# Kernel optimization log

Hardware: AMD Instinct MI355X
Metric: run time of the kernel (lower is better)

The kernel has to match this reference:

```python
import jax, jax.numpy as jnp
import numpy as np
import math

B, S, D_MODEL = 4, 2048, 1024
H, D_HEAD = 16, 64
INIT_RANGE = 0.02


def setup_inputs() -> dict:
    key = jax.random.key(0)
    ks = jax.random.split(key, 10)
    x = jax.random.normal(ks[0], (B, S, D_MODEL), dtype=jnp.float32)
    # torch Linear(in,out): y = x @ W.T + b. We store weights pre-transposed as [H, in, out].
    u = lambda k, shape: jax.random.uniform(k, shape, dtype=jnp.float32, minval=-INIT_RANGE, maxval=INIT_RANGE)
    wq = u(ks[1], (H, D_MODEL, D_HEAD))
    wk = u(ks[2], (H, D_MODEL, D_HEAD))
    wv = u(ks[3], (H, D_MODEL, D_HEAD))
    wo = u(ks[4], (H, D_HEAD, D_MODEL))
    # biases: torch default init is uniform(-1/sqrt(fan_in), 1/sqrt(fan_in)); values don't matter for correctness harness
    bq = u(ks[5], (H, D_HEAD))
    bk = u(ks[6], (H, D_HEAD))
    bv = u(ks[7], (H, D_HEAD))
    bo = u(ks[8], (H, D_MODEL))
    return {"normalized_resid_pre": x, "wq": wq, "bq": bq, "wk": wk, "bk": bk,
            "wv": wv, "bv": bv, "wo": wo, "bo": bo}


def reference(normalized_resid_pre, wq, bq, wk, bk, wv, bv, wo, bo):
    x = normalized_resid_pre  # [B, S, D]
    # Batched multi-head QKV projections (original does a python loop per head)
    q = jnp.einsum('bsd,hde->bhse', x, wq) + bq[None, :, None, :]  # [B,H,S,dh]
    k = jnp.einsum('bsd,hde->bhse', x, wk) + bk[None, :, None, :]
    v = jnp.einsum('bsd,hde->bhse', x, wv) + bv[None, :, None, :]
    scale = 1.0 / math.sqrt(D_HEAD)  # cfg.global_d_head, used unconditionally
    scores = jnp.einsum('bhse,bhte->bhst', q, k) * scale  # [B,H,S,S], non-causal
    attn = jax.nn.softmax(scores, axis=-1)
    heads = jnp.einsum('bhst,bhte->bhse', attn, v)  # [B,H,S,dh]
    # per-head output projections, summed over heads (= sum of per-head Linear outputs)
    out = jnp.einsum('bhse,hed->bsd', heads, wo) + jnp.sum(bo, axis=0)[None, None, :]
    return out
```

## Files before the change

### kernel.cpp

```cpp
#include <hip/hip_runtime.h>
#include <hip/hip_bf16.h>
#include <math.h>


typedef __attribute__((ext_vector_type(8))) short bf16x8;
typedef __attribute__((ext_vector_type(4))) float f32x4;

#define GLDS16(gsrc, lbase) \
    __builtin_amdgcn_global_load_lds((const __attribute__((address_space(1))) void*)(gsrc), \
                                     (__attribute__((address_space(3))) void*)(lbase), 16, 0, 0)

static __device__ __forceinline__ ushort f2bf(float f) {
    unsigned u = __float_as_uint(f);
    u += 0x7fff + ((u >> 16) & 1);
    return (ushort)(u >> 16);
}
static __device__ __forceinline__ float clampf(float v) {
    return fminf(fmaxf(v, -1e30f), 1e30f);
}

__global__ void cvt_x(const float* __restrict__ x, ushort* __restrict__ xb) {
    int idx = blockIdx.x * 256 + threadIdx.x;
    float4 a = ((const float4*)x)[idx * 2];
    float4 b = ((const float4*)x)[idx * 2 + 1];
    uint4 o;
    o.x = (unsigned)f2bf(a.x) | ((unsigned)f2bf(a.y) << 16);
    o.y = (unsigned)f2bf(a.z) | ((unsigned)f2bf(a.w) << 16);
    o.z = (unsigned)f2bf(b.x) | ((unsigned)f2bf(b.y) << 16);
    o.w = (unsigned)f2bf(b.z) | ((unsigned)f2bf(b.w) << 16);
    ((uint4*)xb)[idx] = o;
}

__global__ void pack_wqkv(const float* __restrict__ wq, const float* __restrict__ wk,
                          const float* __restrict__ wv, const float* __restrict__ bq,
                          const float* __restrict__ bk, const float* __restrict__ bv,
                          ushort* __restrict__ WT, float* __restrict__ biasc) {
    int idx = blockIdx.x * 256 + threadIdx.x;
    int k = idx & 1023, n = idx >> 10;
    int proj = n >> 10, he = n & 1023, h = he >> 6, e = he & 63;
    const float* w = (proj == 0) ? wq : (proj == 1) ? wk : wv;
    WT[idx] = f2bf(w[(size_t)h * 65536 + (size_t)k * 64 + e]);
    if (k == 0) {
        const float* bb = (proj == 0) ? bq : (proj == 1) ? bk : bv;
        biasc[n] = bb[he];
    }
}
__global__ void pack_wo(const float* __restrict__ wo, const float* __restrict__ bo,
                        ushort* __restrict__ WoT, float* __restrict__ biaso) {
    int idx = blockIdx.x * 256 + threadIdx.x;
    int he = idx & 1023, d = idx >> 10;
    WoT[idx] = f2bf(wo[(size_t)he * 1024 + d]);
    if (he == 0) {
        float s = 0.f;
        for (int hh = 0; hh < 16; ++hh) s += bo[hh * 1024 + d];
        biaso[d] = s;
    }
}

__global__ __launch_bounds__(256, 2) void gemm_bt(
    const ushort* __restrict__ A, const ushort* __restrict__ Bt,
    const float* __restrict__ bias, ushort* __restrict__ C, ushort* __restrict__ Vt,
    float* __restrict__ Cf, int M, int N, int K, int ldc, int n_split)
{
    __shared__ __align__(16) ushort Al[128][64];
    __shared__ __align__(16) ushort Bl[128][64];
    const int t = threadIdx.x;
    const int lane = t & 63, wave = t >> 6;
    const int wr = wave >> 1, wc = wave & 1;
    const int quad = lane >> 4, l16 = lane & 15;
    const int row0 = blockIdx.x * 128, col0 = blockIdx.y * 128;
    const int sr = t >> 3;
    const int scx = ((t & 7) ^ (sr & 7)) * 8;
    const int xk = l16 & 7;

    f32x4 acc[4][4] = {};

    for (int kt = 0; kt < K; kt += 64) {
        char* abase = (char*)Al + wave * 1024;
        char* bbase = (char*)Bl + wave * 1024;
        const ushort* ag = A  + (size_t)(row0 + sr) * K + kt + scx;
        const ushort* bg = Bt + (size_t)(col0 + sr) * K + kt + scx;
        #pragma unroll
        for (int i = 0; i < 4; ++i) {
            GLDS16(ag + (size_t)i * 32 * K, abase + i * 4096);
            GLDS16(bg + (size_t)i * 32 * K, bbase + i * 4096);
        }
        __syncthreads();
        #pragma unroll
        for (int ks = 0; ks < 2; ++ks) {
            bf16x8 a[4], b[4];
            #pragma unroll
            for (int mi = 0; mi < 4; ++mi)
                a[mi] = *(const bf16x8*)(&Al[wr * 64 + mi * 16 + l16][((ks * 4 + quad) ^ xk) * 8]);
            #pragma unroll
            for (int ni = 0; ni < 4; ++ni)
                b[ni] = *(const bf16x8*)(&Bl[wc * 64 + ni * 16 + l16][((ks * 4 + quad) ^ xk) * 8]);
            #pragma unroll
            for (int mi = 0; mi < 4; ++mi)
                #pragma unroll
                for (int ni = 0; ni < 4; ++ni)
                    acc[mi][ni] = __builtin_amdgcn_mfma_f32_16x16x32_bf16(a[mi], b[ni], acc[mi][ni], 0, 0, 0);
        }
        __syncthreads();
    }
    #pragma unroll
    for (int mi = 0; mi < 4; ++mi) {
        int rowb = row0 + wr * 64 + mi * 16 + quad * 4;
        #pragma unroll
        for (int ni = 0; ni < 4; ++ni) {
            int col = col0 + wc * 64 + ni * 16 + l16;
            float bs = bias ? bias[col] : 0.f;
            #pragma unroll
            for (int r = 0; r < 4; ++r) {
                float v = clampf(acc[mi][ni][r] + bs);
                int row = rowb + r;
                if (Cf) {
                    Cf[(size_t)row * ldc + col] = v;
                } else if (col < n_split) {
                    C[(size_t)row * ldc + col] = f2bf(v);
                } else {
                    int bb = row >> 11, s = row & 2047;
                    Vt[(size_t)bb * (1024 * 2048) + (size_t)(col - n_split) * 2048 + s] = f2bf(v);
                }
            }
        }
    }
}

__global__ __launch_bounds__(256, 2) void attn(
    const ushort* __restrict__ QK, const ushort* __restrict__ Vt, ushort* __restrict__ O)
{
    __shared__ __align__(16) ushort Kl[64][64];
    __shared__ __align__(16) ushort Vl[64][64];
    __shared__ ushort Pl[4][32][76];
    const int qt = blockIdx.x, b = blockIdx.y, h = blockIdx.z;
    const int t = threadIdx.x, lane = t & 63, wave = t >> 6;
    const int quad = lane >> 4, l16 = lane & 15;
    const int rowq0 = b * 2048 + qt * 128 + wave * 32;
    const int sr = t >> 3;
    const int scx = ((t & 7) ^ (sr & 7)) * 8;
    const int xk = l16 & 7;
    const float cscale = 0.125f * 1.44269504088896340736f;
    const float M0 = 14.0f;

    bf16x8 qf[2][2];
    #pragma unroll
    for (int mi = 0; mi < 2; ++mi)
        #pragma unroll
        for (int ks = 0; ks < 2; ++ks)
            qf[mi][ks] = *(const bf16x8*)(QK + (size_t)(rowq0 + mi * 16 + l16) * 2048
                                          + h * 64 + ks * 32 + quad * 8);

    f32x4 of[2][4] = {};
    float lpart[2][4] = {};

    for (int kt = 0; kt < 2048; kt += 64) {
        {
            char* kbase = (char*)Kl + wave * 1024;
            char* vbase = (char*)Vl + wave * 1024;
            const ushort* kg = QK + (size_t)(b * 2048 + kt + sr) * 2048 + 1024 + h * 64 + scx;
            const ushort* vg = Vt + (size_t)b * (1024 * 2048) + (size_t)(h * 64 + sr) * 2048 + kt + scx;
            GLDS16(kg, kbase);
            GLDS16(kg + 32 * 2048, kbase + 4096);
            GLDS16(vg, vbase);
            GLDS16(vg + 32 * 2048, vbase + 4096);
        }
        __syncthreads();

        f32x4 sf[2][4] = {};
        #pragma unroll
        for (int ks = 0; ks < 2; ++ks) {
            bf16x8 kb[4];
            #pragma unroll
            for (int nt = 0; nt < 4; ++nt)
                kb[nt] = *(const bf16x8*)(&Kl[nt * 16 + l16][((ks * 4 + quad) ^ xk) * 8]);
            #pragma unroll
            for (int mi = 0; mi < 2; ++mi)
                #pragma unroll
                for (int nt = 0; nt < 4; ++nt)
                    sf[mi][nt] = __builtin_amdgcn_mfma_f32_16x16x32_bf16(qf[mi][ks], kb[nt], sf[mi][nt], 0, 0, 0);
        }

        #pragma unroll
        for (int mi = 0; mi < 2; ++mi) {
            #pragma unroll
            for (int r = 0; r < 4; ++r) {
                float p0 = exp2f(sf[mi][0][r] * cscale - M0);
                float p1 = exp2f(sf[mi][1][r] * cscale - M0);
                float p2 = exp2f(sf[mi][2][r] * cscale - M0);
                float p3 = exp2f(sf[mi][3][r] * cscale - M0);
                lpart[mi][r] += (p0 + p1) + (p2 + p3);
                int prw = mi * 16 + quad * 4 + r;
                Pl[wave][prw][l16 +  0] = f2bf(p0);
                Pl[wave][prw][l16 + 16] = f2bf(p1);
                Pl[wave][prw][l16 + 32] = f2bf(p2);
                Pl[wave][prw][l16 + 48] = f2bf(p3);
            }
        }

        #pragma unroll
        for (int ks = 0; ks < 2; ++ks) {
            bf16x8 pa[2];
            #pragma unroll
            for (int mi = 0; mi < 2; ++mi)
                pa[mi] = *(const bf16x8*)(&Pl[wave][mi * 16 + l16][ks * 32 + quad * 8]);
            #pragma unroll
            for (int nt = 0; nt < 4; ++nt) {
                bf16x8 vb = *(const bf16x8*)(&Vl[nt * 16 + l16][((ks * 4 + quad) ^ xk) * 8]);
                #pragma unroll
                for (int mi = 0; mi < 2; ++mi)
                    of[mi][nt] = __builtin_amdgcn_mfma_f32_16x16x32_bf16(pa[mi], vb, of[mi][nt], 0, 0, 0);
            }
        }
        __syncthreads();
    }

    #pragma unroll
    for (int mi = 0; mi < 2; ++mi) {
        #pragma unroll
        for (int r = 0; r < 4; ++r) {
            float l = lpart[mi][r];
            #pragma unroll
            for (int d = 1; d < 16; d <<= 1) l += __shfl_xor(l, d, 64);
            float inv = 1.0f / fmaxf(l, 1e-30f);
            int row = rowq0 + mi * 16 + quad * 4 + r;
            #pragma unroll
            for (int nt = 0; nt < 4; ++nt)
                O[(size_t)row * 1024 + h * 64 + nt * 16 + l16] = f2bf(clampf(of[mi][nt][r] * inv));
        }
    }
}

extern "C" void kernel_launch(void* const* d_in, const int* in_sizes, int n_in,
                              void* d_out, int out_size, void* d_ws, size_t ws_size,
                              hipStream_t stream) {
    const float* x  = (const float*)d_in[0];
    const float* wq = (const float*)d_in[1];
    const float* bq = (const float*)d_in[2];
    const float* wk = (const float*)d_in[3];
    const float* bk = (const float*)d_in[4];
    const float* wv = (const float*)d_in[5];
    const float* bv = (const float*)d_in[6];
    const float* wo = (const float*)d_in[7];
    const float* bo = (const float*)d_in[8];

    char* ws = (char*)d_ws;
    const size_t MB = 1024 * 1024;
    ushort* xb    = (ushort*)(ws);
    ushort* WqkvT = (ushort*)(ws + 16 * MB);
    ushort* WoT   = (ushort*)(ws + 22 * MB);
    float*  biasc = (float*) (ws + 24 * MB);
    float*  biaso = (float*) (ws + 24 * MB + 64 * 1024);
    ushort* C1    = (ushort*)(ws + 25 * MB);
    ushort* Vt    = (ushort*)(ws + 57 * MB);
    ushort* Obuf  = (ushort*)(ws + 73 * MB);

    cvt_x    <<<4096, 256, 0, stream>>>(x, xb);
    pack_wqkv<<<(3072 * 1024) / 256, 256, 0, stream>>>(wq, wk, wv, bq, bk, bv, WqkvT, biasc);
    pack_wo  <<<(1024 * 1024) / 256, 256, 0, stream>>>(wo, bo, WoT, biaso);

    gemm_bt<<<dim3(64, 24), 256, 0, stream>>>(xb, WqkvT, biasc, C1, Vt, nullptr,
                                              8192, 3072, 1024, 2048, 2048);
    attn<<<dim3(16, 4, 16), 256, 0, stream>>>(C1, Vt, Obuf);
    gemm_bt<<<dim3(64, 8), 256, 0, stream>>>(Obuf, WoT, biaso, nullptr, nullptr, (float*)d_out,
                                             8192, 1024, 1024, 1024, 0);
}
```

Before: 358.7 us.

## Tile weight packing via LDS, use hardware bf16 cvt, permute V for packed P stores

Rewrites pack_wqkv and pack_wo as 64x64 LDS-tiled transposes so global writes become coalesced 16-byte stores instead of strided scalar writes. f2bf now uses the native __bf16 conversion. The V transpose store is permuted within 64-element groups so each lane in attention can write its four P values as one packed 8-byte LDS store, with the P buffer row stride reduced to 72. The permutation must match the P column order exactly, and the new Pl stride may change bank conflicts.

```diff
diff --git a/kernel.cpp b/kernel.cpp
--- a/kernel.cpp
+++ b/kernel.cpp
@@ -11,9 +11,11 @@
                                      (__attribute__((address_space(3))) void*)(lbase), 16, 0, 0)
 
 static __device__ __forceinline__ ushort f2bf(float f) {
-    unsigned u = __float_as_uint(f);
-    u += 0x7fff + ((u >> 16) & 1);
-    return (ushort)(u >> 16);
+    __bf16 h = (__bf16)f;
+    return *reinterpret_cast<ushort*>(&h);
+}
+static __device__ __forceinline__ unsigned pk_bf16(float a, float b) {
+    return (unsigned)f2bf(a) | ((unsigned)f2bf(b) << 16);
 }
 static __device__ __forceinline__ float clampf(float v) {
     return fminf(fmaxf(v, -1e30f), 1e30f);
@@ -24,10 +26,10 @@
     float4 a = ((const float4*)x)[idx * 2];
     float4 b = ((const float4*)x)[idx * 2 + 1];
     uint4 o;
-    o.x = (unsigned)f2bf(a.x) | ((unsigned)f2bf(a.y) << 16);
-    o.y = (unsigned)f2bf(a.z) | ((unsigned)f2bf(a.w) << 16);
-    o.z = (unsigned)f2bf(b.x) | ((unsigned)f2bf(b.y) << 16);
-    o.w = (unsigned)f2bf(b.z) | ((unsigned)f2bf(b.w) << 16);
+    o.x = pk_bf16(a.x, a.y);
+    o.y = pk_bf16(a.z, a.w);
+    o.z = pk_bf16(b.x, b.y);
+    o.w = pk_bf16(b.z, b.w);
     ((uint4*)xb)[idx] = o;
 }
 
@@ -35,26 +37,49 @@
                           const float* __restrict__ wv, const float* __restrict__ bq,
                           const float* __restrict__ bk, const float* __restrict__ bv,
                           ushort* __restrict__ WT, float* __restrict__ biasc) {
-    int idx = blockIdx.x * 256 + threadIdx.x;
-    int k = idx & 1023, n = idx >> 10;
-    int proj = n >> 10, he = n & 1023, h = he >> 6, e = he & 63;
-    const float* w = (proj == 0) ? wq : (proj == 1) ? wk : wv;
-    WT[idx] = f2bf(w[(size_t)h * 65536 + (size_t)k * 64 + e]);
-    if (k == 0) {
-        const float* bb = (proj == 0) ? bq : (proj == 1) ? bk : bv;
-        biasc[n] = bb[he];
-    }
+    __shared__ __align__(16) ushort Lt[64][72];
+    int bid = blockIdx.x;
+    int kt = bid & 15, h = (bid >> 4) & 15, proj = bid >> 8;
+    const float* w  = (proj == 0) ? wq : (proj == 1) ? wk : wv;
+    const float* bb = (proj == 0) ? bq : (proj == 1) ? bk : bv;
+    int t = threadIdx.x;
+    int e = t & 63, kr = t >> 6;
+    const float* src = w + (size_t)h * 65536 + (size_t)kt * 64 * 64 + e;
+    #pragma unroll
+    for (int i = 0; i < 16; ++i) {
+        int kl = kr * 16 + i;
+        Lt[e][kl] = f2bf(src[(size_t)kl * 64]);
+    }
+    if (kt == 0 && t < 64) biasc[proj * 1024 + h * 64 + t] = bb[h * 64 + t];
+    __syncthreads();
+    int eo = t >> 2, kc = (t & 3) * 16;
+    size_t dst = (size_t)(proj * 1024 + h * 64 + eo) * 1024 + kt * 64 + kc;
+    *(bf16x8*)(WT + dst)     = *(const bf16x8*)(&Lt[eo][kc]);
+    *(bf16x8*)(WT + dst + 8) = *(const bf16x8*)(&Lt[eo][kc + 8]);
 }
 __global__ void pack_wo(const float* __restrict__ wo, const float* __restrict__ bo,
                         ushort* __restrict__ WoT, float* __restrict__ biaso) {
-    int idx = blockIdx.x * 256 + threadIdx.x;
-    int he = idx & 1023, d = idx >> 10;
-    WoT[idx] = f2bf(wo[(size_t)he * 1024 + d]);
-    if (he == 0) {
+    __shared__ __align__(16) ushort Lt[64][72];
+    int bid = blockIdx.x;
+    int het = bid & 15, dt = bid >> 4;
+    int t = threadIdx.x;
+    int dl = t & 63, hw = t >> 6;
+    #pragma unroll
+    for (int i = 0; i < 16; ++i) {
+        int hel = hw * 16 + i;
+        Lt[dl][hel] = f2bf(wo[(size_t)(het * 64 + hel) * 1024 + dt * 64 + dl]);
+    }
+    if (het == 0 && t < 64) {
+        int d = dt * 64 + t;
         float s = 0.f;
         for (int hh = 0; hh < 16; ++hh) s += bo[hh * 1024 + d];
         biaso[d] = s;
     }
+    __syncthreads();
+    int do_ = t >> 2, hc = (t & 3) * 16;
+    size_t dst = (size_t)(dt * 64 + do_) * 1024 + het * 64 + hc;
+    *(bf16x8*)(WoT + dst)     = *(const bf16x8*)(&Lt[do_][hc]);
+    *(bf16x8*)(WoT + dst + 8) = *(const bf16x8*)(&Lt[do_][hc + 8]);
 }
 
 __global__ __launch_bounds__(256, 2) void gemm_bt(
@@ -120,7 +145,8 @@
                     C[(size_t)row * ldc + col] = f2bf(v);
                 } else {
                     int bb = row >> 11, s = row & 2047;
-                    Vt[(size_t)bb * (1024 * 2048) + (size_t)(col - n_split) * 2048 + s] = f2bf(v);
+                    int pos = (s & ~63) | (((s & 15) << 2) | ((s >> 4) & 3));
+                    Vt[(size_t)bb * (1024 * 2048) + (size_t)(col - n_split) * 2048 + pos] = f2bf(v);
                 }
             }
         }
@@ -132,7 +158,7 @@
 {
     __shared__ __align__(16) ushort Kl[64][64];
     __shared__ __align__(16) ushort Vl[64][64];
-    __shared__ ushort Pl[4][32][76];
+    __shared__ __align__(16) ushort Pl[4][32][72];
     const int qt = blockIdx.x, b = blockIdx.y, h = blockIdx.z;
     const int t = threadIdx.x, lane = t & 63, wave = t >> 6;
     const int quad = lane >> 4, l16 = lane & 15;
@@ -191,10 +217,10 @@
                 float p3 = exp2f(sf[mi][3][r] * cscale - M0);
                 lpart[mi][r] += (p0 + p1) + (p2 + p3);
                 int prw = mi * 16 + quad * 4 + r;
-                Pl[wave][prw][l16 +  0] = f2bf(p0);
-                Pl[wave][prw][l16 + 16] = f2bf(p1);
-                Pl[wave][prw][l16 + 32] = f2bf(p2);
-                Pl[wave][prw][l16 + 48] = f2bf(p3);
+                uint2 pk;
+                pk.x = pk_bf16(p0, p1);
+                pk.y = pk_bf16(p2, p3);
+                *(uint2*)(&Pl[wave][prw][l16 * 4]) = pk;
             }
         }
 
@@ -256,8 +282,8 @@
     ushort* Obuf  = (ushort*)(ws + 73 * MB);
 
     cvt_x    <<<4096, 256, 0, stream>>>(x, xb);
-    pack_wqkv<<<(3072 * 1024) / 256, 256, 0, stream>>>(wq, wk, wv, bq, bk, bv, WqkvT, biasc);
-    pack_wo  <<<(1024 * 1024) / 256, 256, 0, stream>>>(wo, bo, WoT, biaso);
+    pack_wqkv<<<768, 256, 0, stream>>>(wq, wk, wv, bq, bk, bv, WqkvT, biasc);
+    pack_wo  <<<256, 256, 0, stream>>>(wo, bo, WoT, biaso);
 
     gemm_bt<<<dim3(64, 24), 256, 0, stream>>>(xb, WqkvT, biasc, C1, Vt, nullptr,
                                               8192, 3072, 1024, 2048, 2048);
```

Result: faster. 343.6 us (-4.2%).
